# Kernel optimization log

Measured on AMD Instinct MI355X. Metric: run time of the kernel, lower is better.

The kernel has to match this reference:

```python
import jax, jax.numpy as jnp
import numpy as np

N = 100000   # nodes
E = 1200000  # edges (avg degree 12)
D = 64       # feature dim (in == hidden == out, forced by residual add)
L = 3        # num_layers


def setup_inputs() -> dict:
    key = jax.random.key(0)
    ks = jax.random.split(key, 8)
    s = 1.0 / np.float32(np.sqrt(D))
    x = jax.random.normal(ks[0], (N, D), jnp.float32)
    edge_index = jax.random.randint(ks[1], (2, E), 0, N, dtype=jnp.int32)
    W1 = jax.random.normal(ks[2], (L, D, D), jnp.float32) * s
    b1 = jnp.zeros((L, D), jnp.float32)
    W2 = jax.random.normal(ks[3], (L, D, D), jnp.float32) * s
    b2 = jnp.zeros((L, D), jnp.float32)
    Wf = jax.random.normal(ks[4], (D, D), jnp.float32) * s
    bf = jnp.zeros((D,), jnp.float32)
    return {"x": x, "edge_index": edge_index, "W1": W1, "b1": b1,
            "W2": W2, "b2": b2, "Wf": Wf, "bf": bf}


def reference(x, edge_index, W1, b1, W2, b2, Wf, bf):
    row, col = edge_index[0], edge_index[1]
    h = x
    for l in range(L):
        def mlp(z):
            # Linear -> ReLU -> Linear (same MLP applied to messages and combine)
            return jnp.maximum(z @ W1[l] + b1[l], 0.0) @ W2[l] + b2[l]
        msgs = mlp(h[col])                                        # [E, D] gather + MLP
        agg = jax.ops.segment_sum(msgs, row, num_segments=N)      # [N, D] scatter-add
        h = mlp(h + agg)                                          # residual combine + MLP
    return h @ Wf + bf
```

## Files before the change

kernel.cpp:

```cpp
#include <hip/hip_runtime.h>

typedef unsigned int uint;
typedef unsigned short ushort;
typedef __attribute__((ext_vector_type(8))) short short8;
typedef __attribute__((ext_vector_type(4))) float f32x4;

#define DIM 64
#define MAXDEG 48
#define NBUCKET 8

__device__ __forceinline__ ushort f2bf(float f) {
    uint u = __float_as_uint(f);
    u += 0x7fffu + ((u >> 16) & 1u);
    return (ushort)(u >> 16);
}
__device__ __forceinline__ float bf2f(ushort h) {
    return __uint_as_float(((uint)h) << 16);
}

__global__ __launch_bounds__(256) void f32_to_bf16(
    const float4* __restrict__ in, ushort4* __restrict__ out, int n4)
{
    int i = blockIdx.x * blockDim.x + threadIdx.x;
    if (i >= n4) return;
    float4 v = in[i];
    ushort4 o;
    o.x = f2bf(v.x); o.y = f2bf(v.y); o.z = f2bf(v.z); o.w = f2bf(v.w);
    out[i] = o;
}

__global__ __launch_bounds__(256) void mlp_mfma(
    const ushort* __restrict__ in, ushort* __restrict__ out,
    const float* __restrict__ W1, const float* __restrict__ b1,
    const float* __restrict__ W2, const float* __restrict__ b2,
    int ntiles)
{
    __shared__ __align__(16) ushort lds[4][16 * 72];
    const int lane = threadIdx.x & 63;
    const int wid  = threadIdx.x >> 6;
    const int c = lane & 15, g = lane >> 4;
    ushort* myl = &lds[wid][0];

    short8 wf[2][2][2][4];
#pragma unroll
    for (int kc = 0; kc < 2; ++kc)
#pragma unroll
        for (int t = 0; t < 4; ++t)
#pragma unroll
            for (int j = 0; j < 8; ++j) {
                float w1v = W1[(kc * 32 + g * 8 + j) * 64 + t * 16 + c];
                float w2v = W2[(kc * 32 + g * 8 + j) * 64 + t * 16 + c];
                ushort h1 = f2bf(w1v); ushort l1 = f2bf(w1v - bf2f(h1));
                ushort h2 = f2bf(w2v); ushort l2 = f2bf(w2v - bf2f(h2));
                wf[0][0][kc][t][j] = (short)h1; wf[0][1][kc][t][j] = (short)l1;
                wf[1][0][kc][t][j] = (short)h2; wf[1][1][kc][t][j] = (short)l2;
            }
    float bc1[4], bc2[4];
#pragma unroll
    for (int t = 0; t < 4; ++t) { bc1[t] = b1[t * 16 + c]; bc2[t] = b2[t * 16 + c]; }

    const int gw = (int)((blockIdx.x * blockDim.x + threadIdx.x) >> 6);
    const int nw = (int)((gridDim.x * blockDim.x) >> 6);

    for (int tile = gw; tile < ntiles; tile += nw) {
        const ushort* rp = in + (size_t)(tile * 16 + c) * DIM;
        short8 a0 = *(const short8*)(rp + g * 8);
        short8 a1 = *(const short8*)(rp + 32 + g * 8);

        f32x4 acc[4];
#pragma unroll
        for (int t = 0; t < 4; ++t) {
            f32x4 z = {0.f, 0.f, 0.f, 0.f};
            z = __builtin_amdgcn_mfma_f32_16x16x32_bf16(a0, wf[0][0][0][t], z, 0, 0, 0);
            z = __builtin_amdgcn_mfma_f32_16x16x32_bf16(a1, wf[0][0][1][t], z, 0, 0, 0);
            z = __builtin_amdgcn_mfma_f32_16x16x32_bf16(a0, wf[0][1][0][t], z, 0, 0, 0);
            z = __builtin_amdgcn_mfma_f32_16x16x32_bf16(a1, wf[0][1][1][t], z, 0, 0, 0);
            acc[t] = z;
        }
#pragma unroll
        for (int t = 0; t < 4; ++t)
#pragma unroll
            for (int r = 0; r < 4; ++r) {
                float v = fmaxf(acc[t][r] + bc1[t], 0.f);
                myl[(4 * g + r) * 72 + 16 * t + c] = f2bf(v);
            }
        short8 h0 = *(const short8*)(myl + c * 72 + g * 8);
        short8 h1 = *(const short8*)(myl + c * 72 + 32 + g * 8);

#pragma unroll
        for (int t = 0; t < 4; ++t) {
            f32x4 z = {0.f, 0.f, 0.f, 0.f};
            z = __builtin_amdgcn_mfma_f32_16x16x32_bf16(h0, wf[1][0][0][t], z, 0, 0, 0);
            z = __builtin_amdgcn_mfma_f32_16x16x32_bf16(h1, wf[1][0][1][t], z, 0, 0, 0);
            z = __builtin_amdgcn_mfma_f32_16x16x32_bf16(h0, wf[1][1][0][t], z, 0, 0, 0);
            z = __builtin_amdgcn_mfma_f32_16x16x32_bf16(h1, wf[1][1][1][t], z, 0, 0, 0);
#pragma unroll
            for (int r = 0; r < 4; ++r)
                out[(size_t)(tile * 16 + 4 * g + r) * DIM + 16 * t + c] = f2bf(z[r] + bc2[t]);
        }
    }
}

__global__ __launch_bounds__(256) void linear_mfma(
    const ushort* __restrict__ in, float* __restrict__ out,
    const float* __restrict__ Wg, const float* __restrict__ bg, int ntiles)
{
    const int lane = threadIdx.x & 63;
    const int c = lane & 15, g = lane >> 4;

    short8 wf[2][2][4];
#pragma unroll
    for (int kc = 0; kc < 2; ++kc)
#pragma unroll
        for (int t = 0; t < 4; ++t)
#pragma unroll
            for (int j = 0; j < 8; ++j) {
                float wv = Wg[(kc * 32 + g * 8 + j) * 64 + t * 16 + c];
                ushort h = f2bf(wv); ushort l = f2bf(wv - bf2f(h));
                wf[0][kc][t][j] = (short)h; wf[1][kc][t][j] = (short)l;
            }
    float bc[4];
#pragma unroll
    for (int t = 0; t < 4; ++t) bc[t] = bg[t * 16 + c];

    const int gw = (int)((blockIdx.x * blockDim.x + threadIdx.x) >> 6);
    const int nw = (int)((gridDim.x * blockDim.x) >> 6);

    for (int tile = gw; tile < ntiles; tile += nw) {
        const ushort* rp = in + (size_t)(tile * 16 + c) * DIM;
        short8 a0 = *(const short8*)(rp + g * 8);
        short8 a1 = *(const short8*)(rp + 32 + g * 8);
#pragma unroll
        for (int t = 0; t < 4; ++t) {
            f32x4 z = {0.f, 0.f, 0.f, 0.f};
            z = __builtin_amdgcn_mfma_f32_16x16x32_bf16(a0, wf[0][0][t], z, 0, 0, 0);
            z = __builtin_amdgcn_mfma_f32_16x16x32_bf16(a1, wf[0][1][t], z, 0, 0, 0);
            z = __builtin_amdgcn_mfma_f32_16x16x32_bf16(a0, wf[1][0][t], z, 0, 0, 0);
            z = __builtin_amdgcn_mfma_f32_16x16x32_bf16(a1, wf[1][1][t], z, 0, 0, 0);
#pragma unroll
            for (int r = 0; r < 4; ++r)
                out[(size_t)(tile * 16 + 4 * g + r) * DIM + 16 * t + c] = z[r] + bc[t];
        }
    }
}

__global__ __launch_bounds__(256) void fill_ell_bucketed(
    const int* __restrict__ rowi, const int* __restrict__ coli,
    int* __restrict__ cnt, int* __restrict__ ell, int E, int nper)
{
    const int bucket = blockIdx.x & (NBUCKET - 1);
    const int bpb = gridDim.x / NBUCKET;
    const int bidx = blockIdx.x >> 3;
    const int lo = bucket * nper;
    const int hi = lo + nper;
    const int stride = bpb * 256;
    const int e4n = E >> 2;

    for (int i = bidx * 256 + threadIdx.x; i < e4n; i += stride) {
        int4 r4 = ((const int4*)rowi)[i];
        int4 c4 = ((const int4*)coli)[i];
#pragma unroll
        for (int u = 0; u < 4; ++u) {
            int r = (u == 0) ? r4.x : (u == 1) ? r4.y : (u == 2) ? r4.z : r4.w;
            if (r >= lo && r < hi) {
                int c = (u == 0) ? c4.x : (u == 1) ? c4.y : (u == 2) ? c4.z : c4.w;
                int slot = atomicAdd(&cnt[r], 1);
                if (slot < MAXDEG) ell[(size_t)r * MAXDEG + slot] = c;
            }
        }
    }
}

__global__ __launch_bounds__(256) void gather_kernel(
    const ushort* __restrict__ m, const ushort* __restrict__ h,
    const int* __restrict__ ell, const int* __restrict__ cnt,
    ushort* __restrict__ t, int N)
{
    const int lane = threadIdx.x & 63;
    const int node = (int)((blockIdx.x * blockDim.x + threadIdx.x) >> 6);
    if (node >= N) return;
    int deg = cnt[node];
    deg = deg < MAXDEG ? deg : MAXDEG;
    const int* el = ell + (size_t)node * MAXDEG;
    float a0 = bf2f(h[(size_t)node * DIM + lane]);
    float a1 = 0.f, a2 = 0.f, a3 = 0.f;
    int i = 0;
    for (; i + 4 <= deg; i += 4) {
        int4 q = *(const int4*)(el + i);
        a0 += bf2f(m[(size_t)q.x * DIM + lane]);
        a1 += bf2f(m[(size_t)q.y * DIM + lane]);
        a2 += bf2f(m[(size_t)q.z * DIM + lane]);
        a3 += bf2f(m[(size_t)q.w * DIM + lane]);
    }
    for (; i < deg; ++i)
        a0 += bf2f(m[(size_t)el[i] * DIM + lane]);
    t[(size_t)node * DIM + lane] = f2bf((a0 + a1) + (a2 + a3));
}

extern "C" void kernel_launch(void* const* d_in, const int* in_sizes, int n_in,
                              void* d_out, int out_size, void* d_ws, size_t ws_size,
                              hipStream_t stream)
{
    const float* x  = (const float*)d_in[0];
    const int*   ei = (const int*)d_in[1];
    const float* W1 = (const float*)d_in[2];
    const float* b1 = (const float*)d_in[3];
    const float* W2 = (const float*)d_in[4];
    const float* b2 = (const float*)d_in[5];
    const float* Wf = (const float*)d_in[6];
    const float* bf = (const float*)d_in[7];
    float* out = (float*)d_out;

    const int N = in_sizes[0] / DIM;
    const int E = in_sizes[1] / 2;
    const int NT = N / 16;

    ushort* hA = (ushort*)d_ws;
    ushort* hB = hA + (size_t)N * DIM;
    ushort* hC = hB + (size_t)N * DIM;
    int* cnt = (int*)(hC + (size_t)N * DIM);
    int* ell = cnt + N;

    f32_to_bf16<<<(N * DIM / 4 + 255) / 256, 256, 0, stream>>>(
        (const float4*)x, (ushort4*)hA, N * DIM / 4);
    hipMemsetAsync(cnt, 0, (size_t)N * sizeof(int), stream);
    fill_ell_bucketed<<<2048, 256, 0, stream>>>(
        ei, ei + E, cnt, ell, E, (N + NBUCKET - 1) / NBUCKET);

    for (int l = 0; l < 3; ++l) {
        const float* w1  = W1 + (size_t)l * DIM * DIM;
        const float* w2  = W2 + (size_t)l * DIM * DIM;
        const float* bb1 = b1 + (size_t)l * DIM;
        const float* bb2 = b2 + (size_t)l * DIM;
        mlp_mfma<<<512, 256, 0, stream>>>(hA, hB, w1, bb1, w2, bb2, NT);
        gather_kernel<<<(N * 64 + 255) / 256, 256, 0, stream>>>(hB, hA, ell, cnt, hC, N);
        mlp_mfma<<<512, 256, 0, stream>>>(hC, hA, w1, bb1, w2, bb2, NT);
    }
    linear_mfma<<<512, 256, 0, stream>>>(hA, out, Wf, bf, NT);
}
```

Baseline: 406.9 us.

## Drop split-bf16 weight correction, widen gather unroll, enlarge grids

Weights in the MLP kernel are now converted to a single bf16 value instead of a hi/lo pair, which halves the MFMA count and the weight registers. The gather loop unrolls to eight independent accumulators so more loads are in flight. Grid sizes for the MLP, final linear and ELL fill kernels are doubled, and launch bounds ask for higher occupancy. Dropping the low-order weight term lowers numerical accuracy against the fp32 reference.

```diff
diff --git a/kernel.cpp b/kernel.cpp
--- a/kernel.cpp
+++ b/kernel.cpp
@@ -29,7 +29,7 @@
     out[i] = o;
 }
 
-__global__ __launch_bounds__(256) void mlp_mfma(
+__global__ __launch_bounds__(256, 4) void mlp_mfma(
     const ushort* __restrict__ in, ushort* __restrict__ out,
     const float* __restrict__ W1, const float* __restrict__ b1,
     const float* __restrict__ W2, const float* __restrict__ b2,
@@ -41,19 +41,15 @@
     const int c = lane & 15, g = lane >> 4;
     ushort* myl = &lds[wid][0];
 
-    short8 wf[2][2][2][4];
+    short8 wf[2][2][4];
 #pragma unroll
     for (int kc = 0; kc < 2; ++kc)
 #pragma unroll
         for (int t = 0; t < 4; ++t)
 #pragma unroll
             for (int j = 0; j < 8; ++j) {
-                float w1v = W1[(kc * 32 + g * 8 + j) * 64 + t * 16 + c];
-                float w2v = W2[(kc * 32 + g * 8 + j) * 64 + t * 16 + c];
-                ushort h1 = f2bf(w1v); ushort l1 = f2bf(w1v - bf2f(h1));
-                ushort h2 = f2bf(w2v); ushort l2 = f2bf(w2v - bf2f(h2));
-                wf[0][0][kc][t][j] = (short)h1; wf[0][1][kc][t][j] = (short)l1;
-                wf[1][0][kc][t][j] = (short)h2; wf[1][1][kc][t][j] = (short)l2;
+                wf[0][kc][t][j] = (short)f2bf(W1[(kc * 32 + g * 8 + j) * 64 + t * 16 + c]);
+                wf[1][kc][t][j] = (short)f2bf(W2[(kc * 32 + g * 8 + j) * 64 + t * 16 + c]);
             }
     float bc1[4], bc2[4];
 #pragma unroll
@@ -71,10 +67,8 @@
 #pragma unroll
         for (int t = 0; t < 4; ++t) {
             f32x4 z = {0.f, 0.f, 0.f, 0.f};
-            z = __builtin_amdgcn_mfma_f32_16x16x32_bf16(a0, wf[0][0][0][t], z, 0, 0, 0);
-            z = __builtin_amdgcn_mfma_f32_16x16x32_bf16(a1, wf[0][0][1][t], z, 0, 0, 0);
-            z = __builtin_amdgcn_mfma_f32_16x16x32_bf16(a0, wf[0][1][0][t], z, 0, 0, 0);
-            z = __builtin_amdgcn_mfma_f32_16x16x32_bf16(a1, wf[0][1][1][t], z, 0, 0, 0);
+            z = __builtin_amdgcn_mfma_f32_16x16x32_bf16(a0, wf[0][0][t], z, 0, 0, 0);
+            z = __builtin_amdgcn_mfma_f32_16x16x32_bf16(a1, wf[0][1][t], z, 0, 0, 0);
             acc[t] = z;
         }
 #pragma unroll
@@ -90,10 +84,8 @@
 #pragma unroll
         for (int t = 0; t < 4; ++t) {
             f32x4 z = {0.f, 0.f, 0.f, 0.f};
-            z = __builtin_amdgcn_mfma_f32_16x16x32_bf16(h0, wf[1][0][0][t], z, 0, 0, 0);
-            z = __builtin_amdgcn_mfma_f32_16x16x32_bf16(h1, wf[1][0][1][t], z, 0, 0, 0);
-            z = __builtin_amdgcn_mfma_f32_16x16x32_bf16(h0, wf[1][1][0][t], z, 0, 0, 0);
-            z = __builtin_amdgcn_mfma_f32_16x16x32_bf16(h1, wf[1][1][1][t], z, 0, 0, 0);
+            z = __builtin_amdgcn_mfma_f32_16x16x32_bf16(h0, wf[1][0][t], z, 0, 0, 0);
+            z = __builtin_amdgcn_mfma_f32_16x16x32_bf16(h1, wf[1][1][t], z, 0, 0, 0);
 #pragma unroll
             for (int r = 0; r < 4; ++r)
                 out[(size_t)(tile * 16 + 4 * g + r) * DIM + 16 * t + c] = f2bf(z[r] + bc2[t]);
@@ -182,19 +174,34 @@
     int deg = cnt[node];
     deg = deg < MAXDEG ? deg : MAXDEG;
     const int* el = ell + (size_t)node * MAXDEG;
+
     float a0 = bf2f(h[(size_t)node * DIM + lane]);
-    float a1 = 0.f, a2 = 0.f, a3 = 0.f;
+    float a1 = 0.f, a2 = 0.f, a3 = 0.f, a4 = 0.f, a5 = 0.f, a6 = 0.f, a7 = 0.f;
     int i = 0;
-    for (; i + 4 <= deg; i += 4) {
+    for (; i + 8 <= deg; i += 8) {
+        int4 q0 = *(const int4*)(el + i);
+        int4 q1 = *(const int4*)(el + i + 4);
+        a0 += bf2f(m[(size_t)q0.x * DIM + lane]);
+        a1 += bf2f(m[(size_t)q0.y * DIM + lane]);
+        a2 += bf2f(m[(size_t)q0.z * DIM + lane]);
+        a3 += bf2f(m[(size_t)q0.w * DIM + lane]);
+        a4 += bf2f(m[(size_t)q1.x * DIM + lane]);
+        a5 += bf2f(m[(size_t)q1.y * DIM + lane]);
+        a6 += bf2f(m[(size_t)q1.z * DIM + lane]);
+        a7 += bf2f(m[(size_t)q1.w * DIM + lane]);
+    }
+    if (i + 4 <= deg) {
         int4 q = *(const int4*)(el + i);
         a0 += bf2f(m[(size_t)q.x * DIM + lane]);
         a1 += bf2f(m[(size_t)q.y * DIM + lane]);
         a2 += bf2f(m[(size_t)q.z * DIM + lane]);
         a3 += bf2f(m[(size_t)q.w * DIM + lane]);
+        i += 4;
     }
     for (; i < deg; ++i)
         a0 += bf2f(m[(size_t)el[i] * DIM + lane]);
-    t[(size_t)node * DIM + lane] = f2bf((a0 + a1) + (a2 + a3));
+    t[(size_t)node * DIM + lane] =
+        f2bf(((a0 + a1) + (a2 + a3)) + ((a4 + a5) + (a6 + a7)));
 }
 
 extern "C" void kernel_launch(void* const* d_in, const int* in_sizes, int n_in,
@@ -224,7 +231,7 @@
     f32_to_bf16<<<(N * DIM / 4 + 255) / 256, 256, 0, stream>>>(
         (const float4*)x, (ushort4*)hA, N * DIM / 4);
     hipMemsetAsync(cnt, 0, (size_t)N * sizeof(int), stream);
-    fill_ell_bucketed<<<2048, 256, 0, stream>>>(
+    fill_ell_bucketed<<<4096, 256, 0, stream>>>(
         ei, ei + E, cnt, ell, E, (N + NBUCKET - 1) / NBUCKET);
 
     for (int l = 0; l < 3; ++l) {
@@ -232,9 +239,9 @@
         const float* w2  = W2 + (size_t)l * DIM * DIM;
         const float* bb1 = b1 + (size_t)l * DIM;
         const float* bb2 = b2 + (size_t)l * DIM;
-        mlp_mfma<<<512, 256, 0, stream>>>(hA, hB, w1, bb1, w2, bb2, NT);
+        mlp_mfma<<<1024, 256, 0, stream>>>(hA, hB, w1, bb1, w2, bb2, NT);
         gather_kernel<<<(N * 64 + 255) / 256, 256, 0, stream>>>(hB, hA, ell, cnt, hC, N);
-        mlp_mfma<<<512, 256, 0, stream>>>(hC, hA, w1, bb1, w2, bb2, NT);
-    }
-    linear_mfma<<<512, 256, 0, stream>>>(hA, out, Wf, bf, NT);
-}
+        mlp_mfma<<<1024, 256, 0, stream>>>(hC, hA, w1, bb1, w2, bb2, NT);
+    }
+    linear_mfma<<<1024, 256, 0, stream>>>(hA, out, Wf, bf, NT);
+}
```

New measurement: 354.9 us. -12.8%, faster.
